# Optimization experiments

Measured on AMD Instinct MI355X. Metric: run time of the kernel, lower is better.

The kernel has to match this reference:

```python
import jax, jax.numpy as jnp
import numpy as np

D_MODEL, D_STATE, D_CONV, D_INNER, DT_RANK, K = 96, 16, 3, 192, 6, 4
B, H, W = 1, 64, 64


def setup_inputs() -> dict:
    key = jax.random.key(0)
    ks = jax.random.split(key, 10)
    x = jax.random.normal(ks[0], (B, H, W, D_MODEL), jnp.float32)
    in_proj_w = jax.random.normal(ks[1], (2 * D_INNER, D_MODEL), jnp.float32) * 0.02
    conv_w = jax.random.normal(ks[2], (D_INNER, 1, D_CONV, D_CONV), jnp.float32) * 0.1
    conv_b = jnp.zeros((D_INNER,), jnp.float32)
    x_proj_w = jax.random.normal(ks[3], (K, DT_RANK + 2 * D_STATE, D_INNER), jnp.float32) * 0.02
    dt_std = DT_RANK ** -0.5
    dt_w = jax.random.uniform(ks[4], (K, D_INNER, DT_RANK), jnp.float32, -dt_std, dt_std)
    # dt bias init: inv-softplus of dt ~ logUniform(1e-3, 1e-1)
    u = jax.random.uniform(ks[5], (K, D_INNER), jnp.float32)
    dt = jnp.exp(u * (np.log(0.1) - np.log(0.001)) + np.log(0.001)).clip(1e-4)
    dt_b = dt + jnp.log(-jnp.expm1(-dt))
    A_logs = jnp.log(jnp.broadcast_to(jnp.arange(1, D_STATE + 1, dtype=jnp.float32), (K * D_INNER, D_STATE)))
    Ds = jnp.ones((K * D_INNER,), jnp.float32)
    ln_g = jnp.ones((D_INNER,), jnp.float32)
    ln_b = jnp.zeros((D_INNER,), jnp.float32)
    out_proj_w = jax.random.normal(ks[6], (D_MODEL, D_INNER), jnp.float32) * 0.02
    return dict(x=x, in_proj_w=in_proj_w, conv_w=conv_w, conv_b=conv_b, x_proj_w=x_proj_w,
                dt_w=dt_w, dt_b=dt_b, A_logs=A_logs, Ds=Ds, ln_g=ln_g, ln_b=ln_b,
                out_proj_w=out_proj_w)


def _ss2d(x, in_proj_w, conv_w, conv_b, x_proj_w, dt_w, dt_b, A_logs, Ds, ln_g, ln_b, out_proj_w):
    b, h, w, c = x.shape
    L = h * w
    d = conv_w.shape[0]            # d_inner
    n = A_logs.shape[1]            # d_state
    r = dt_w.shape[2]              # dt_rank
    # in_proj + split
    xz = jnp.einsum('bhwc,ec->bhwe', x, in_proj_w)
    xx, z = xz[..., :d], xz[..., d:]
    # depthwise conv (NCHW) + SiLU
    xc = xx.transpose(0, 3, 1, 2)
    pad = (D_CONV - 1) // 2
    xc = jax.lax.conv_general_dilated(xc, conv_w, (1, 1), [(pad, pad), (pad, pad)],
                                      feature_group_count=d) + conv_b[None, :, None, None]
    xc = jax.nn.silu(xc)
    # 4 scan directions: HW, WH, and their reverses
    x_hw = xc.reshape(b, d, L)
    x_wh = xc.transpose(0, 1, 3, 2).reshape(b, d, L)
    xs = jnp.stack([x_hw, x_wh, x_hw[..., ::-1], x_wh[..., ::-1]], axis=1)  # (b,K,d,L)
    x_dbl = jnp.einsum('bkdl,kcd->bkcl', xs, x_proj_w)
    dts, Bs, Cs = x_dbl[:, :, :r], x_dbl[:, :, r:r + n], x_dbl[:, :, r + n:]
    dts = jnp.einsum('bkrl,kdr->bkdl', dts, dt_w)
    delta = jax.nn.softplus(dts + dt_b[None, :, :, None])        # (b,K,d,L)
    A = -jnp.exp(A_logs).reshape(K, d, n)
    # time-major scanned inputs
    dA = jnp.exp(jnp.einsum('bkdl,kdn->lbkdn', delta, A))        # (L,b,K,d,n)
    dBu = jnp.einsum('bkdl,bknl,bkdl->lbkdn', delta, Bs, xs)
    Ct = Cs.transpose(3, 0, 1, 2)                                # (L,b,K,n)
    def step(hst, inp):
        dA_t, dBu_t, C_t = inp
        hst = dA_t * hst + dBu_t
        return hst, jnp.einsum('bkdn,bkn->bkd', hst, C_t)
    h0 = jnp.zeros((b, K, d, n), jnp.float32)
    _, ys = jax.lax.scan(step, h0, (dA, dBu, Ct))                # ys: (L,b,K,d)
    out_y = ys.transpose(1, 2, 3, 0) + xs * Ds.reshape(K, d)[None, :, :, None]
    # recombine directions
    inv = out_y[:, 2:4][..., ::-1]
    y1 = out_y[:, 0]
    y2 = inv[:, 0]
    wh = out_y[:, 1].reshape(b, d, w, h).transpose(0, 1, 3, 2).reshape(b, d, L)
    invwh = inv[:, 1].reshape(b, d, w, h).transpose(0, 1, 3, 2).reshape(b, d, L)
    y = (y1 + y2 + wh + invwh).transpose(0, 2, 1).reshape(b, h, w, d)
    # LayerNorm (eps=1e-5, torch default)
    mu = y.mean(-1, keepdims=True)
    var = ((y - mu) ** 2).mean(-1, keepdims=True)
    y = (y - mu) * jax.lax.rsqrt(var + 1e-5) * ln_g + ln_b
    y = y * jax.nn.silu(z)
    return jnp.einsum('bhwd,cd->bhwc', y, out_proj_w)


def reference(x, in_proj_w, conv_w, conv_b, x_proj_w, dt_w, dt_b, A_logs, Ds, ln_g, ln_b, out_proj_w):
    return _ss2d(x, in_proj_w, conv_w, conv_b, x_proj_w, dt_w, dt_b, A_logs, Ds, ln_g, ln_b, out_proj_w)
```

## Files before the change

kernel.cpp:

```cpp
#include <hip/hip_runtime.h>
#include <hip/hip_bf16.h>

#define LL 4096
#define DM 96
#define DI 192
#define NS 16
#define RK 6
#define RKP 8
#define KD 4
#define CPROJ 38
#define NCH (KD*DI)
#define NC (KD*DI*NS)
#define PT 32
#define WS 196
#define OT 8
#define L2E 1.44269504f

__device__ __forceinline__ float bf2f(unsigned short u){
  unsigned int x = ((unsigned int)u) << 16;
  return __uint_as_float(x);
}
__device__ __forceinline__ float b2f(__hip_bfloat16 v){ return __bfloat162float(v); }

__device__ __forceinline__ void detect_bf16(const unsigned short* __restrict__ xh, int tid, int* sflag){
  if (tid < 64){
    unsigned short u = xh[2*tid];
    int e = (u >> 7) & 0xFF;
    int sane = (e >= 107 && e <= 131) ? 1 : 0;
    unsigned long long m = __ballot(sane);
    if (tid == 0) *sflag = (__popcll(m) >= 32) ? 1 : 0;
  }
}

__device__ __forceinline__ int dir_map(int k, int t){
  if (k==0) return t;
  if (k==1) return ((t&63)<<6) | (t>>6);
  if (k==2) return 4095 - t;
  int u = 4095 - t; return ((u&63)<<6) | (u>>6);
}

struct P12 { const void* p[12]; };

__global__ void __launch_bounds__(384) k_inprojcvt(P12 ptrs, float* __restrict__ cvt,
                         float* __restrict__ xx, float* __restrict__ z) {
  __shared__ float xr[8*DM];
  __shared__ int sflag;
  int tid = threadIdx.x;
  detect_bf16((const unsigned short*)ptrs.p[0], tid, &sflag);
  __syncthreads();
  int f = sflag;
  if (blockIdx.x >= LL/8){
    const int off[12] = {0,36864,38592,38784,67968,72576,73344,85632,86400,86592,86784,105216};
    int i = (blockIdx.x - LL/8)*384 + tid + 36864;
    if (i < 105216){
      int j = 1;
      #pragma unroll
      for (int s = 2; s < 11; s++) if (i >= off[s]) j = s;
      int e = i - off[j];
      const void* src = ptrs.p[j+1];
      cvt[i] = f ? b2f(((const __hip_bfloat16*)src)[e]) : ((const float*)src)[e];
    }
    return;
  }
  int l0 = blockIdx.x * 8;
  if (f){
    const __hip_bfloat16* xb = (const __hip_bfloat16*)ptrs.p[0] + (size_t)l0*DM;
    for (int i = tid; i < 8*DM; i += 384) xr[i] = b2f(xb[i]);
  } else {
    const float* xf = (const float*)ptrs.p[0] + (size_t)l0*DM;
    for (int i = tid; i < 8*DM; i += 384) xr[i] = xf[i];
  }
  __syncthreads();
  int e = tid;
  float acc[8];
  #pragma unroll
  for (int i=0;i<8;i++) acc[i]=0.f;
  const float4* xr4 = (const float4*)xr;
  if (f){
    const ushort4* wb = (const ushort4*)((const unsigned short*)ptrs.p[1] + (size_t)e*DM);
    #pragma unroll 4
    for (int c4=0;c4<DM/4;c4++){
      ushort4 uv = wb[c4];
      float4 wv = make_float4(bf2f(uv.x), bf2f(uv.y), bf2f(uv.z), bf2f(uv.w));
      #pragma unroll
      for (int i=0;i<8;i++){
        float4 xv = xr4[i*24 + c4];
        acc[i] = fmaf(wv.x,xv.x,fmaf(wv.y,xv.y,fmaf(wv.z,xv.z,fmaf(wv.w,xv.w,acc[i]))));
      }
    }
  } else {
    const float4* wr4 = (const float4*)((const float*)ptrs.p[1] + (size_t)e*DM);
    #pragma unroll 4
    for (int c4=0;c4<DM/4;c4++){
      float4 wv = wr4[c4];
      #pragma unroll
      for (int i=0;i<8;i++){
        float4 xv = xr4[i*24 + c4];
        acc[i] = fmaf(wv.x,xv.x,fmaf(wv.y,xv.y,fmaf(wv.z,xv.z,fmaf(wv.w,xv.w,acc[i]))));
      }
    }
  }
  if (e < DI) {
    #pragma unroll
    for (int i=0;i<8;i++) xx[(l0+i)*DI + e] = acc[i];
  } else {
    int e2 = e - DI;
    #pragma unroll
    for (int i=0;i<8;i++) z[(l0+i)*DI + e2] = acc[i];
  }
}

__global__ void k_conv(const float* __restrict__ xx,
                       const float* __restrict__ cw,
                       const float* __restrict__ cb,
                       float* __restrict__ xc) {
  int l = blockIdx.x;
  int d = threadIdx.x;
  int h = l >> 6, w = l & 63;
  float acc = cb[d];
  #pragma unroll
  for (int ki=0; ki<3; ki++){
    int hh = h + ki - 1;
    if ((unsigned)hh >= 64u) continue;
    #pragma unroll
    for (int kj=0;kj<3;kj++){
      int wj = w + kj - 1;
      if ((unsigned)wj >= 64u) continue;
      acc = fmaf(cw[d*9 + ki*3 + kj], xx[(hh*64+wj)*DI + d], acc);
    }
  }
  float v = acc / (1.f + __expf(-acc));
  xc[l*DI + d] = v;
}

__global__ void __launch_bounds__(256) k_proj(const float* __restrict__ xc,
                       const float* __restrict__ xpw,
                       float* __restrict__ dts,
                       float* __restrict__ Bb, float* __restrict__ Cb) {
  __shared__ float wl[CPROJ*WS];
  __shared__ float xs[PT*WS];
  int b = blockIdx.x;
  int k = b >> 7;
  int t_base = (b & 127) * PT;
  int tid = threadIdx.x;
  for (int idx = tid; idx < CPROJ*DI; idx += 256){
    int cc = idx / DI, j = idx - cc*DI;
    wl[cc*WS + j] = xpw[(k*CPROJ + cc)*DI + j];
  }
  for (int idx = tid; idx < PT*DI; idx += 256){
    int tt = idx / DI, j = idx - tt*DI;
    xs[tt*WS + j] = xc[dir_map(k, t_base + tt)*DI + j];
  }
  __syncthreads();
  int tg = tid & 7;
  int ty = tid >> 3;
  int cc0 = ty;
  int has2 = (ty + 32 < CPROJ);
  int cc1 = has2 ? (ty + 32) : ty;
  float a0x=0.f,a0y=0.f,a0z=0.f,a0w=0.f;
  float a1x=0.f,a1y=0.f,a1z=0.f,a1w=0.f;
  const float4* w0p = (const float4*)&wl[cc0*WS];
  const float4* w1p = (const float4*)&wl[cc1*WS];
  const float4* x0p = (const float4*)&xs[(tg     )*WS];
  const float4* x1p = (const float4*)&xs[(tg +  8)*WS];
  const float4* x2p = (const float4*)&xs[(tg + 16)*WS];
  const float4* x3p = (const float4*)&xs[(tg + 24)*WS];
  #pragma unroll 4
  for (int jc = 0; jc < DI/4; jc++){
    float4 w0 = w0p[jc], w1 = w1p[jc];
    float4 x0 = x0p[jc], x1 = x1p[jc], x2 = x2p[jc], x3 = x3p[jc];
    a0x = fmaf(w0.x,x0.x,fmaf(w0.y,x0.y,fmaf(w0.z,x0.z,fmaf(w0.w,x0.w,a0x))));
    a0y = fmaf(w0.x,x1.x,fmaf(w0.y,x1.y,fmaf(w0.z,x1.z,fmaf(w0.w,x1.w,a0y))));
    a0z = fmaf(w0.x,x2.x,fmaf(w0.y,x2.y,fmaf(w0.z,x2.z,fmaf(w0.w,x2.w,a0z))));
    a0w = fmaf(w0.x,x3.x,fmaf(w0.y,x3.y,fmaf(w0.z,x3.z,fmaf(w0.w,x3.w,a0w))));
    a1x = fmaf(w1.x,x0.x,fmaf(w1.y,x0.y,fmaf(w1.z,x0.z,fmaf(w1.w,x0.w,a1x))));
    a1y = fmaf(w1.x,x1.x,fmaf(w1.y,x1.y,fmaf(w1.z,x1.z,fmaf(w1.w,x1.w,a1y))));
    a1z = fmaf(w1.x,x2.x,fmaf(w1.y,x2.y,fmaf(w1.z,x2.z,fmaf(w1.w,x2.w,a1z))));
    a1w = fmaf(w1.x,x3.x,fmaf(w1.y,x3.y,fmaf(w1.z,x3.z,fmaf(w1.w,x3.w,a1w))));
  }
  float accs0[4] = {a0x,a0y,a0z,a0w};
  float accs1[4] = {a1x,a1y,a1z,a1w};
  #pragma unroll
  for (int i=0;i<4;i++){
    int t = t_base + tg + 8*i;
    size_t kt = (size_t)k*LL + t;
    {
      int cc = cc0; float v = accs0[i];
      if (cc < RK)            dts[kt*RKP + cc] = v;
      else if (cc < RK+NS)    Bb [kt*NS + (cc-RK)] = v;
      else                    Cb [kt*NS + (cc-RK-NS)] = v;
    }
    if (has2){
      int cc = ty + 32; float v = accs1[i];
      if (cc < RK+NS)         Bb [kt*NS + (cc-RK)] = v;
      else                    Cb [kt*NS + (cc-RK-NS)] = v;
    }
  }
}

template<int CHB>
__global__ void __launch_bounds__(192) k_scanA(
                      const float* __restrict__ xc,
                      const float* __restrict__ dts,
                      const float* __restrict__ Bbuf,
                      const float* __restrict__ A_logs,
                      const float* __restrict__ dtw,
                      const float* __restrict__ dtb,
                      float* __restrict__ cumDbuf,
                      float* __restrict__ Harr) {
  constexpr int CS = LL >> CHB;
  __shared__ float ds_[CS*RKP];
  __shared__ float Bs[CS*NS];
  int b = blockIdx.x;
  int k = b >> CHB;
  int c = b & ((1<<CHB)-1);
  int t0 = c*CS;
  int d = threadIdx.x;
  int kd = k*DI + d;
  for (int i = d; i < CS*RKP; i += 192) ds_[i] = dts[((size_t)k*LL + t0)*RKP + i];
  for (int i = d; i < CS*NS;  i += 192) Bs[i]  = Bbuf[((size_t)k*LL + t0)*NS + i];
  float bt = dtb[kd];
  float w0 = dtw[kd*RK+0], w1 = dtw[kd*RK+1], w2 = dtw[kd*RK+2];
  float w3 = dtw[kd*RK+3], w4 = dtw[kd*RK+4], w5 = dtw[kd*RK+5];
  float A2[16], h[16];
  {
    const float4* ap = (const float4*)&A_logs[kd*NS];
    #pragma unroll
    for (int i=0;i<4;i++){
      float4 av = ap[i];
      A2[4*i+0] = -__expf(av.x)*L2E; A2[4*i+1] = -__expf(av.y)*L2E;
      A2[4*i+2] = -__expf(av.z)*L2E; A2[4*i+3] = -__expf(av.w)*L2E;
    }
  }
  #pragma unroll
  for (int n=0;n<16;n++) h[n] = 0.f;
  __syncthreads();
  float cumD = 0.f;
  #pragma unroll 2
  for (int s=0; s<CS; s++){
    float4 lo = *(const float4*)(ds_ + s*RKP);
    float4 hi = *(const float4*)(ds_ + s*RKP + 4);
    float v = bt;
    v = fmaf(w0, lo.x, v); v = fmaf(w1, lo.y, v); v = fmaf(w2, lo.z, v);
    v = fmaf(w3, lo.w, v); v = fmaf(w4, hi.x, v); v = fmaf(w5, hi.y, v);
    float sp = (v > 20.f) ? v : __logf(1.f + __expf(v));
    cumD += sp;
    int row = dir_map(k, t0 + s);
    float sx = sp * xc[(size_t)row*DI + d];
    float4 b0 = *(const float4*)(Bs + s*NS);
    float4 b1 = *(const float4*)(Bs + s*NS + 4);
    float4 b2 = *(const float4*)(Bs + s*NS + 8);
    float4 b3 = *(const float4*)(Bs + s*NS + 12);
    float bb[16] = {b0.x,b0.y,b0.z,b0.w, b1.x,b1.y,b1.z,b1.w,
                    b2.x,b2.y,b2.z,b2.w, b3.x,b3.y,b3.z,b3.w};
    #pragma unroll
    for (int n=0;n<16;n++){
      float a = exp2f(sp*A2[n]);
      h[n] = fmaf(a, h[n], sx*bb[n]);
    }
  }
  cumDbuf[(size_t)c*NCH + kd] = cumD;
  float4* hp = (float4*)(Harr + ((size_t)c*NCH + kd)*16);
  hp[0] = make_float4(h[0],h[1],h[2],h[3]);
  hp[1] = make_float4(h[4],h[5],h[6],h[7]);
  hp[2] = make_float4(h[8],h[9],h[10],h[11]);
  hp[3] = make_float4(h[12],h[13],h[14],h[15]);
}

template<int CHB>
__global__ void __launch_bounds__(256) k_scan2(const float* __restrict__ A_logs,
                                               const float* __restrict__ cumDbuf,
                                               float* __restrict__ Harr) {
  constexpr int CH = 1 << CHB;
  int idx = blockIdx.x*256 + threadIdx.x;
  int kd = idx >> 4;
  float A2 = -__expf(A_logs[idx]) * L2E;
  float h = 0.f;
  #pragma unroll 4
  for (int c=0;c<CH;c++){
    float hl = Harr[(size_t)c*NC + idx];
    float P = exp2f(A2 * cumDbuf[(size_t)c*NCH + kd]);
    Harr[(size_t)c*NC + idx] = h;
    h = fmaf(P, h, hl);
  }
}

template<int CHB>
__global__ void __launch_bounds__(192) k_scanB(
                      const float* __restrict__ xc,
                      const float* __restrict__ dts,
                      const float* __restrict__ Bbuf,
                      const float* __restrict__ Cbuf,
                      const float* __restrict__ A_logs,
                      const float* __restrict__ dtw,
                      const float* __restrict__ dtb,
                      const float* __restrict__ Harr,
                      float* __restrict__ ydir) {
  constexpr int CS = LL >> CHB;
  __shared__ float ds_[CS*RKP];
  __shared__ float Bs[CS*NS];
  __shared__ float Cs[CS*NS];
  int b = blockIdx.x;
  int k = b >> CHB;
  int c = b & ((1<<CHB)-1);
  int t0 = c*CS;
  int d = threadIdx.x;
  int kd = k*DI + d;
  for (int i = d; i < CS*RKP; i += 192) ds_[i] = dts[((size_t)k*LL + t0)*RKP + i];
  for (int i = d; i < CS*NS;  i += 192) Bs[i]  = Bbuf[((size_t)k*LL + t0)*NS + i];
  for (int i = d; i < CS*NS;  i += 192) Cs[i]  = Cbuf[((size_t)k*LL + t0)*NS + i];
  float bt = dtb[kd];
  float w0 = dtw[kd*RK+0], w1 = dtw[kd*RK+1], w2 = dtw[kd*RK+2];
  float w3 = dtw[kd*RK+3], w4 = dtw[kd*RK+4], w5 = dtw[kd*RK+5];
  float A2[16], h[16];
  {
    const float4* ap = (const float4*)&A_logs[kd*NS];
    #pragma unroll
    for (int i=0;i<4;i++){
      float4 av = ap[i];
      A2[4*i+0] = -__expf(av.x)*L2E; A2[4*i+1] = -__expf(av.y)*L2E;
      A2[4*i+2] = -__expf(av.z)*L2E; A2[4*i+3] = -__expf(av.w)*L2E;
    }
  }
  {
    const float4* hp = (const float4*)(Harr + ((size_t)c*NCH + kd)*16);
    float4 h0 = hp[0], h1 = hp[1], h2 = hp[2], h3 = hp[3];
    h[0]=h0.x; h[1]=h0.y; h[2]=h0.z; h[3]=h0.w;
    h[4]=h1.x; h[5]=h1.y; h[6]=h1.z; h[7]=h1.w;
    h[8]=h2.x; h[9]=h2.y; h[10]=h2.z; h[11]=h2.w;
    h[12]=h3.x; h[13]=h3.y; h[14]=h3.z; h[15]=h3.w;
  }
  __syncthreads();
  #pragma unroll 2
  for (int s=0; s<CS; s++){
    float4 lo = *(const float4*)(ds_ + s*RKP);
    float4 hi = *(const float4*)(ds_ + s*RKP + 4);
    float v = bt;
    v = fmaf(w0, lo.x, v); v = fmaf(w1, lo.y, v); v = fmaf(w2, lo.z, v);
    v = fmaf(w3, lo.w, v); v = fmaf(w4, hi.x, v); v = fmaf(w5, hi.y, v);
    float sp = (v > 20.f) ? v : __logf(1.f + __expf(v));
    int row = dir_map(k, t0 + s);
    float sx = sp * xc[(size_t)row*DI + d];
    float4 b0 = *(const float4*)(Bs + s*NS);
    float4 b1 = *(const float4*)(Bs + s*NS + 4);
    float4 b2 = *(const float4*)(Bs + s*NS + 8);
    float4 b3 = *(const float4*)(Bs + s*NS + 12);
    float bb[16] = {b0.x,b0.y,b0.z,b0.w, b1.x,b1.y,b1.z,b1.w,
                    b2.x,b2.y,b2.z,b2.w, b3.x,b3.y,b3.z,b3.w};
    #pragma unroll
    for (int n=0;n<16;n++){
      float a = exp2f(sp*A2[n]);
      h[n] = fmaf(a, h[n], sx*bb[n]);
    }
    float4 c0 = *(const float4*)(Cs + s*NS);
    float4 c1 = *(const float4*)(Cs + s*NS + 4);
    float4 c2 = *(const float4*)(Cs + s*NS + 8);
    float4 c3 = *(const float4*)(Cs + s*NS + 12);
    float cc[16] = {c0.x,c0.y,c0.z,c0.w, c1.x,c1.y,c1.z,c1.w,
                    c2.x,c2.y,c2.z,c2.w, c3.x,c3.y,c3.z,c3.w};
    float y0=0.f, y1=0.f, y2=0.f, y3=0.f;
    #pragma unroll
    for (int n=0;n<4;n++){
      y0 = fmaf(h[4*n+0], cc[4*n+0], y0);
      y1 = fmaf(h[4*n+1], cc[4*n+1], y1);
      y2 = fmaf(h[4*n+2], cc[4*n+2], y2);
      y3 = fmaf(h[4*n+3], cc[4*n+3], y3);
    }
    ydir[((size_t)k*LL + row)*DI + d] = (y0+y1)+(y2+y3);
  }
}

__global__ void __launch_bounds__(192) k_out(
                      const float* __restrict__ ydir,
                      const float* __restrict__ xc,
                      const float* __restrict__ z,
                      const float* __restrict__ Ds,
                      const float* __restrict__ ln_g,
                      const float* __restrict__ ln_b,
                      const float* __restrict__ opw,
                      void* __restrict__ out,
                      const unsigned short* __restrict__ xh) {
  __shared__ float gs[OT*WS];
  __shared__ float ps[2][OT][24];
  __shared__ float mv[2][OT];
  __shared__ int sflag;
  int tid = threadIdx.x;
  int d = tid;
  detect_bf16(xh, tid, &sflag);
  int l0 = blockIdx.x * OT;
  float dsum = Ds[d] + Ds[DI+d] + Ds[2*DI+d] + Ds[3*DI+d];
  #pragma unroll
  for (int r=0;r<OT;r++){
    size_t ld = (size_t)(l0+r)*DI + d;
    float y = ydir[ld]
            + ydir[(size_t)LL*DI   + ld]
            + ydir[(size_t)2*LL*DI + ld]
            + ydir[(size_t)3*LL*DI + ld];
    gs[r*WS + d] = fmaf(xc[ld], dsum, y);
  }
  __syncthreads();
  {
    int r = tid / 24, lane = tid - r*24;
    float s1 = 0.f, s2 = 0.f;
    #pragma unroll
    for (int j = lane; j < DI; j += 24){
      float v = gs[r*WS + j];
      s1 += v; s2 += v*v;
    }
    ps[0][r][lane] = s1; ps[1][r][lane] = s2;
  }
  __syncthreads();
  if (tid < OT){
    float a = 0.f, bb = 0.f;
    #pragma unroll
    for (int j=0;j<24;j++){ a += ps[0][tid][j]; bb += ps[1][tid][j]; }
    float mu = a * (1.f/192.f);
    float var = bb * (1.f/192.f) - mu*mu;
    mv[0][tid] = mu; mv[1][tid] = rsqrtf(var + 1e-5f);
  }
  __syncthreads();
  float lg = ln_g[d], lb = ln_b[d];
  #pragma unroll
  for (int r=0;r<OT;r++){
    float yn = (gs[r*WS + d] - mv[0][r]) * mv[1][r] * lg + lb;
    float zv = z[(size_t)(l0+r)*DI + d];
    gs[r*WS + d] = yn * (zv / (1.f + __expf(-zv)));
  }
  __syncthreads();
  int half = tid / 96;
  int e = tid - half*96;
  int r0 = half*4;
  float acc[4];
  #pragma unroll
  for (int i=0;i<4;i++) acc[i] = 0.f;
  const float4* wrow = (const float4*)(opw + e*DI);
  #pragma unroll 4
  for (int jc = 0; jc < DI/4; jc++){
    float4 w = wrow[jc];
    #pragma unroll
    for (int i=0;i<4;i++){
      float4 gv = *(const float4*)&gs[(r0+i)*WS + jc*4];
      acc[i] = fmaf(w.x,gv.x,fmaf(w.y,gv.y,fmaf(w.z,gv.z,fmaf(w.w,gv.w,acc[i]))));
    }
  }
  int f = sflag;
  #pragma unroll
  for (int i=0;i<4;i++){
    int l = l0 + r0 + i;
    if (f) ((__hip_bfloat16*)out)[l*DM + e] = __float2bfloat16(acc[i]);
    else   ((float*)out)[l*DM + e] = acc[i];
  }
}

extern "C" void kernel_launch(void* const* d_in, const int* in_sizes, int n_in,
                              void* d_out, int out_size, void* d_ws, size_t ws_size,
                              hipStream_t stream) {
  float* ws = (float*)d_ws;
  float* cvt = ws + 16;
  const int off[12] = {0,36864,38592,38784,67968,72576,73344,85632,86400,86592,86784,105216};
  float* c[12];
  c[0] = nullptr;
  for (int i = 1; i < 12; i++) c[i] = cvt + off[i-1];

  float* xx   = cvt + 105216;
  float* z    = xx + (size_t)LL*DI;
  float* xc   = z  + (size_t)LL*DI;
  float* dts  = xc + (size_t)LL*DI;
  float* Bb   = dts + (size_t)KD*LL*RKP;
  float* Cb   = Bb + (size_t)KD*LL*NS;
  float* cumD = Cb + (size_t)KD*LL*NS;

  size_t fixed = 16 + 105216 + 3*(size_t)LL*DI + (size_t)KD*LL*RKP
               + 2*(size_t)KD*LL*NS + (size_t)KD*LL*DI;
  size_t need8 = (fixed + 256*(size_t)(NCH + NC)) * 4;
  int chBits = (ws_size >= need8) ? 8 : 6;
  int CHn = 1 << chBits;
  float* Harr = cumD + (size_t)CHn*NCH;
  float* ydir = Harr + (size_t)CHn*NC;

  P12 ptrs;
  for (int i = 0; i < 12; i++) ptrs.p[i] = d_in[i];

  k_inprojcvt<<<LL/8 + 178, 384, 0, stream>>>(ptrs, cvt, xx, z);
  k_conv<<<LL, DI, 0, stream>>>(xx, c[2], c[3], xc);
  k_proj<<<KD*(LL/PT), 256, 0, stream>>>(xc, c[4], dts, Bb, Cb);
  if (chBits == 8){
    k_scanA<8><<<KD*256, 192, 0, stream>>>(xc, dts, Bb, c[7], c[5], c[6], cumD, Harr);
    k_scan2<8><<<NC/256, 256, 0, stream>>>(c[7], cumD, Harr);
    k_scanB<8><<<KD*256, 192, 0, stream>>>(xc, dts, Bb, Cb, c[7], c[5], c[6], Harr, ydir);
  } else {
    k_scanA<6><<<KD*64, 192, 0, stream>>>(xc, dts, Bb, c[7], c[5], c[6], cumD, Harr);
    k_scan2<6><<<NC/256, 256, 0, stream>>>(c[7], cumD, Harr);
    k_scanB<6><<<KD*64, 192, 0, stream>>>(xc, dts, Bb, Cb, c[7], c[5], c[6], Harr, ydir);
  }
  k_out<<<LL/OT, 192, 0, stream>>>(ydir, xc, z, c[8], c[9], c[10], c[11], d_out,
                                   (const unsigned short*)d_in[0]);
}
```

Before: 220.1 us.

## Stage chunk-carry scan through LDS with coalesced float4 loads and more blocks

The inter-chunk carry scan previously ran one thread per state element, each stepping serially through global memory, spread over only a few dozen blocks. Each block now bulk-loads a 64-state by all-chunks tile of Harr and the matching cumD values into shared memory using coalesced float4 accesses. It then runs the serial recurrence from LDS on 64 threads and writes the tile back coalesced. This spreads the traffic over four times as many blocks and takes global latency out of the serial loop, at the cost of roughly 70KB of LDS per block, which limits occupancy.

```diff
diff --git a/kernel.cpp b/kernel.cpp
--- a/kernel.cpp
+++ b/kernel.cpp
@@ -268,20 +268,46 @@
 }
 
 template<int CHB>
-__global__ void __launch_bounds__(256) k_scan2(const float* __restrict__ A_logs,
+__global__ void __launch_bounds__(512) k_scan2(const float* __restrict__ A_logs,
                                                const float* __restrict__ cumDbuf,
                                                float* __restrict__ Harr) {
   constexpr int CH = 1 << CHB;
-  int idx = blockIdx.x*256 + threadIdx.x;
-  int kd = idx >> 4;
-  float A2 = -__expf(A_logs[idx]) * L2E;
-  float h = 0.f;
-  #pragma unroll 4
-  for (int c=0;c<CH;c++){
-    float hl = Harr[(size_t)c*NC + idx];
-    float P = exp2f(A2 * cumDbuf[(size_t)c*NCH + kd]);
-    Harr[(size_t)c*NC + idx] = h;
-    h = fmaf(P, h, hl);
+  constexpr int CHP = CH + 1;
+  __shared__ float hs[64][CHP];
+  __shared__ float cds[4][CH];
+  int tid = threadIdx.x;
+  int base = blockIdx.x * 64;
+  int kd0 = blockIdx.x * 4;
+  for (int i4 = tid; i4 < 16*CH; i4 += 512){
+    int c = i4 >> 4;
+    int jv = (i4 & 15) * 4;
+    float4 v = *(const float4*)&Harr[(size_t)c*NC + base + jv];
+    hs[jv][c] = v.x; hs[jv+1][c] = v.y; hs[jv+2][c] = v.z; hs[jv+3][c] = v.w;
+  }
+  for (int i = tid; i < 4*CH; i += 512){
+    int c = i >> 2, kdl = i & 3;
+    cds[kdl][c] = cumDbuf[(size_t)c*NCH + kd0 + kdl];
+  }
+  __syncthreads();
+  if (tid < 64){
+    float A2 = -__expf(A_logs[base + tid]) * L2E;
+    const float* cd = cds[tid >> 4];
+    float* hr = hs[tid];
+    float h = 0.f;
+    #pragma unroll 4
+    for (int c = 0; c < CH; c++){
+      float hl = hr[c];
+      float P = exp2f(A2 * cd[c]);
+      hr[c] = h;
+      h = fmaf(P, h, hl);
+    }
+  }
+  __syncthreads();
+  for (int i4 = tid; i4 < 16*CH; i4 += 512){
+    int c = i4 >> 4;
+    int jv = (i4 & 15) * 4;
+    float4 v = make_float4(hs[jv][c], hs[jv+1][c], hs[jv+2][c], hs[jv+3][c]);
+    *(float4*)&Harr[(size_t)c*NC + base + jv] = v;
   }
 }
 
@@ -486,11 +512,11 @@
   k_proj<<<KD*(LL/PT), 256, 0, stream>>>(xc, c[4], dts, Bb, Cb);
   if (chBits == 8){
     k_scanA<8><<<KD*256, 192, 0, stream>>>(xc, dts, Bb, c[7], c[5], c[6], cumD, Harr);
-    k_scan2<8><<<NC/256, 256, 0, stream>>>(c[7], cumD, Harr);
+    k_scan2<8><<<NCH/4, 512, 0, stream>>>(c[7], cumD, Harr);
     k_scanB<8><<<KD*256, 192, 0, stream>>>(xc, dts, Bb, Cb, c[7], c[5], c[6], Harr, ydir);
   } else {
     k_scanA<6><<<KD*64, 192, 0, stream>>>(xc, dts, Bb, c[7], c[5], c[6], cumD, Harr);
-    k_scan2<6><<<NC/256, 256, 0, stream>>>(c[7], cumD, Harr);
+    k_scan2<6><<<NCH/4, 512, 0, stream>>>(c[7], cumD, Harr);
     k_scanB<6><<<KD*64, 192, 0, stream>>>(xc, dts, Bb, Cb, c[7], c[5], c[6], Harr, ydir);
   }
   k_out<<<LL/OT, 192, 0, stream>>>(ydir, xc, z, c[8], c[9], c[10], c[11], d_out,
```

Result: faster. 200.0 us (-9.1%).
